# Kernel tuning notes

Hardware: AMD Instinct MI355X
Metric: run time of the kernel (lower is better)

Reference implementation:

```python
import jax, jax.numpy as jnp
import numpy as np

SCALE = 10.0
DIM = 512
DIM_HEAD = 64
HEADS = DIM // DIM_HEAD
LN_EPS = 1e-05
L2_EPS = 1e-12


def l2norm(t, axis=1):
    # Faithful to source: default axis=1 (token axis for [b, n, h, d] tensors)
    denom = jnp.clip(jnp.linalg.norm(t, ord=2, axis=axis, keepdims=True), L2_EPS)
    return t / denom


def setup_inputs() -> dict:
    key = jax.random.key(0)
    k1, k2, k3 = jax.random.split(key, 3)
    B, H, W, C = 8, 32, 32, 512
    x = jax.random.normal(k1, (B, H, W, C), dtype=jnp.float32)
    ln_scale = jnp.ones((C,), dtype=jnp.float32)
    # 1x1 convs == channel matmuls; fan-in scaled init
    w_qkv = jax.random.normal(k2, (C, 3 * DIM), dtype=jnp.float32) / np.sqrt(C)
    w_out = jax.random.normal(k3, (DIM, C), dtype=jnp.float32) / np.sqrt(DIM)
    b_out = jnp.zeros((C,), dtype=jnp.float32)
    return {"x": x, "ln_scale": ln_scale, "w_qkv": w_qkv, "w_out": w_out, "b_out": b_out}


def reference(x, ln_scale, w_qkv, w_out, b_out):
    B, H, W, C = x.shape
    N = H * W
    # LayerNorm over channels (use_bias=False, use_scale=True)
    mean = jnp.mean(x, axis=-1, keepdims=True)
    var = jnp.mean(jnp.square(x - mean), axis=-1, keepdims=True)
    y = (x - mean) * jax.lax.rsqrt(var + LN_EPS) * ln_scale
    # 1x1 conv QKV projection (no bias)
    qkv = jnp.einsum('bhwc,cf->bhwf', y, w_qkv)  # [B,H,W,3*DIM]
    q, k, v = jnp.split(qkv, 3, axis=-1)
    # b x y (h d) -> b (x y) h d
    def to_tokens(t):
        return t.reshape(B, N, HEADS, DIM_HEAD)
    q, k, v = map(to_tokens, (q, k, v))
    # l2norm over axis=1 (token axis), faithful to source default
    q = l2norm(q)
    k = l2norm(k)
    sim = jnp.einsum('bihd,bjhd->bhij', q, k) * SCALE  # [B,heads,N,N]
    attn = jax.nn.softmax(sim, axis=-1)
    out = jnp.einsum('bhij,bjhd->bhid', attn, v)  # [B,heads,N,d]
    # b h (x y) d -> b x y (h d)
    out = out.transpose(0, 2, 1, 3).reshape(B, H, W, HEADS * DIM_HEAD)
    # 1x1 output conv (with bias)
    out = jnp.einsum('bhwf,fc->bhwc', out, w_out) + b_out
    return out
```

## Files before the change

kernel.cpp:

```cpp
#include <hip/hip_runtime.h>

typedef __bf16 bf16x8 __attribute__((ext_vector_type(8)));
typedef float f32x4 __attribute__((ext_vector_type(4)));
typedef float f32x16 __attribute__((ext_vector_type(16)));

#define DEV static __device__ __forceinline__

DEV unsigned short f2bf(float f) {
    union { __bf16 h; unsigned short s; } c; c.h = (__bf16)f; return c.s;
}
DEV float bf2f(unsigned short h) {
    union { unsigned u; float f; } c; c.u = ((unsigned)h) << 16; return c.f;
}
DEV unsigned packbf2(float a, float b) {
    union { __bf16 h[2]; unsigned u; } c;
    c.h[0] = (__bf16)a; c.h[1] = (__bf16)b; return c.u;
}

DEV f32x4 mfma16(bf16x8 a, bf16x8 b, f32x4 c) {
    return __builtin_amdgcn_mfma_f32_16x16x32_bf16(a, b, c, 0, 0, 0);
}
DEV f32x16 mfma32(bf16x8 a, bf16x8 b, f32x16 c) {
    return __builtin_amdgcn_mfma_f32_32x32x16_bf16(a, b, c, 0, 0, 0);
}

#define GLOAD16(gp, lp)                                                        \
    __builtin_amdgcn_global_load_lds(                                          \
        (const __attribute__((address_space(1))) unsigned int*)(gp),           \
        (__attribute__((address_space(3))) unsigned int*)(lp), 16, 0, 0)

#define BARRIER_PINNED()                                                       \
    __builtin_amdgcn_s_barrier();                                              \
    __builtin_amdgcn_sched_barrier(0)

__global__ __launch_bounds__(256) void ln_conv_kernel(const float* __restrict__ x,
                                                      const float* __restrict__ lnsc,
                                                      unsigned short* __restrict__ y,
                                                      float* __restrict__ ssq,
                                                      const float* __restrict__ wqkv,
                                                      const float* __restrict__ wout,
                                                      unsigned short* __restrict__ wqkvt,
                                                      unsigned short* __restrict__ woutt) {
    const int t = threadIdx.x;
    if (blockIdx.x >= 2048) {
        __shared__ __bf16 tile[64][65];
        const int wblk = blockIdx.x - 2048;
        const float* src;
        unsigned short* dst;
        int ldsrc, k0, f0;
        if (wblk < 192) {
            src = wqkv; dst = wqkvt; ldsrc = 1536;
            k0 = (wblk / 24) * 64; f0 = (wblk % 24) * 64;
        } else {
            int w2 = wblk - 192;
            src = wout; dst = woutt; ldsrc = 512;
            k0 = (w2 >> 3) * 64; f0 = (w2 & 7) * 64;
        }
#pragma unroll
        for (int j = 0; j < 16; j++) {
            int idx = t + j * 256;
            int a = idx >> 6, b2 = idx & 63;
            tile[b2][a] = (__bf16)src[(size_t)(k0 + a) * ldsrc + f0 + b2];
        }
        __syncthreads();
#pragma unroll
        for (int j = 0; j < 16; j++) {
            int idx = t + j * 256;
            int fb = idx >> 6, kc = idx & 63;
            union { __bf16 h; unsigned short s; } cv;
            cv.h = tile[fb][kc];
            dst[(size_t)(f0 + fb) * 512 + k0 + kc] = cv.s;
        }
        return;
    }
    if (blockIdx.x < 32) ssq[(blockIdx.x << 8) | t] = 0.0f;
    const int token = blockIdx.x * 4 + (t >> 6);
    const int lane = t & 63;
    const float4* xp = (const float4*)(x + (size_t)token * 512 + lane * 8);
    float4 v0 = xp[0], v1 = xp[1];
    float s = v0.x + v0.y + v0.z + v0.w + v1.x + v1.y + v1.z + v1.w;
    float s2 = v0.x * v0.x + v0.y * v0.y + v0.z * v0.z + v0.w * v0.w +
               v1.x * v1.x + v1.y * v1.y + v1.z * v1.z + v1.w * v1.w;
#pragma unroll
    for (int off = 1; off < 64; off <<= 1) {
        s += __shfl_xor(s, off);
        s2 += __shfl_xor(s2, off);
    }
    const float mean = s * (1.0f / 512.0f);
    const float var = s2 * (1.0f / 512.0f) - mean * mean;
    const float rstd = rsqrtf(var + 1e-5f);
    const float4* sp = (const float4*)(lnsc + lane * 8);
    float4 sc0 = sp[0], sc1 = sp[1];
    union { __bf16 h[8]; uint4 v; } pk;
    pk.h[0] = (__bf16)((v0.x - mean) * rstd * sc0.x);
    pk.h[1] = (__bf16)((v0.y - mean) * rstd * sc0.y);
    pk.h[2] = (__bf16)((v0.z - mean) * rstd * sc0.z);
    pk.h[3] = (__bf16)((v0.w - mean) * rstd * sc0.w);
    pk.h[4] = (__bf16)((v1.x - mean) * rstd * sc1.x);
    pk.h[5] = (__bf16)((v1.y - mean) * rstd * sc1.y);
    pk.h[6] = (__bf16)((v1.z - mean) * rstd * sc1.z);
    pk.h[7] = (__bf16)((v1.w - mean) * rstd * sc1.w);
    *(uint4*)(y + (size_t)token * 512 + lane * 8) = pk.v;
}

template <int WM, int WN, int BK, int NCOLS, bool OUT_BF16, bool BIAS, bool QKV,
          bool DB>
__global__ __launch_bounds__(256) void gemm_bt(const unsigned short* __restrict__ A,
                                               const unsigned short* __restrict__ Bt,
                                               void* __restrict__ Cout,
                                               const float* __restrict__ bias,
                                               float* __restrict__ ssq,
                                               unsigned short* __restrict__ kst,
                                               unsigned short* __restrict__ vst,
                                               int M, int K) {
    constexpr int BM = 2 * WM, BN = 2 * WN;
    constexpr int RB = BK * 2;
    constexpr int RMASK = BK / 8 - 1;
    constexpr int ASZ = BM * RB, BSZ = BN * RB;
    constexpr int NLA = ASZ / 4096, NLB = BSZ / 4096;
    constexpr int MI = WM / 16, NI = WN / 16;
    constexpr int NBUF = DB ? 2 : 1;
    constexpr int STG = NBUF * (ASZ + BSZ);
    constexpr int TTB = QKV ? 128 * 136 * 2 : 0;
    constexpr int LDSB = STG > TTB ? STG : TTB;
    __shared__ __align__(16) char smem[LDSB];
    const int t = threadIdx.x;
    const int w = t >> 6, lane = t & 63;
    const int g = lane >> 4, l15 = lane & 15;
    const int wr = w >> 1, wc = w & 1;
    const int bR = blockIdx.x, bC = blockIdx.y;
    f32x4 acc[MI][NI] = {};
    const size_t ldb = (size_t)K * 2;
    const char* Ag = (const char*)A + (size_t)bR * BM * ldb;
    const char* Bg = (const char*)Bt + (size_t)bC * BN * ldb;

#define GSTAGE(buf, kt_)                                                            \
    {                                                                               \
        char* Ad = smem + (buf) * (ASZ + BSZ);                                      \
        char* Bd = Ad + ASZ;                                                        \
        _Pragma("unroll") for (int i = 0; i < NLA; i++) {                           \
            int o = i * 4096 + t * 16;                                              \
            int row = o / RB, kb = (o % RB) ^ ((row & RMASK) << 4);                 \
            GLOAD16(Ag + (size_t)row * ldb + (size_t)(kt_) * 2 + kb, Ad + o);       \
        }                                                                           \
        _Pragma("unroll") for (int i = 0; i < NLB; i++) {                           \
            int o = i * 4096 + t * 16;                                              \
            int row = o / RB, kb = (o % RB) ^ ((row & RMASK) << 4);                 \
            GLOAD16(Bg + (size_t)row * ldb + (size_t)(kt_) * 2 + kb, Bd + o);       \
        }                                                                           \
    }

#define GCOMPUTE(buf)                                                               \
    {                                                                               \
        const char* Ab = smem + (buf) * (ASZ + BSZ);                                \
        const char* Bb = Ab + ASZ;                                                  \
        _Pragma("unroll") for (int kk = 0; kk < BK; kk += 32) {                     \
            bf16x8 a[MI], bb[NI];                                                   \
            _Pragma("unroll") for (int m = 0; m < MI; m++) {                        \
                int row = wr * WM + m * 16 + l15;                                   \
                int kb = ((kk + g * 8) * 2) ^ ((row & RMASK) << 4);                 \
                a[m] = *(const bf16x8*)(Ab + row * RB + kb);                        \
            }                                                                       \
            _Pragma("unroll") for (int n = 0; n < NI; n++) {                        \
                int row = wc * WN + n * 16 + l15;                                   \
                int kb = ((kk + g * 8) * 2) ^ ((row & RMASK) << 4);                 \
                bb[n] = *(const bf16x8*)(Bb + row * RB + kb);                       \
            }                                                                       \
            _Pragma("unroll") for (int m = 0; m < MI; m++)                          \
                _Pragma("unroll") for (int n = 0; n < NI; n++)                      \
                    acc[m][n] = mfma16(a[m], bb[n], acc[m][n]);                     \
        }                                                                           \
    }

    const int NT = K / BK;
    if constexpr (DB) {
        GSTAGE(0, 0)
        for (int tt = 0; tt < NT; ++tt) {
            const int cur = tt & 1;
            if (tt + 1 < NT) {
                GSTAGE(cur ^ 1, (tt + 1) * BK)
                asm volatile("s_waitcnt vmcnt(%0)" ::"n"(NLA + NLB) : "memory");
            } else {
                asm volatile("s_waitcnt vmcnt(0)" ::: "memory");
            }
            BARRIER_PINNED();
            GCOMPUTE(cur)
            BARRIER_PINNED();
        }
    } else {
        for (int tt = 0; tt < NT; ++tt) {
            __syncthreads();
            GSTAGE(0, tt * BK)
            asm volatile("s_waitcnt vmcnt(0)" ::: "memory");
            __syncthreads();
            GCOMPUTE(0)
        }
    }
#undef GSTAGE
#undef GCOMPUTE

    const int rbase = bR * BM + wr * WM;
    const int cbase = bC * BN + wc * WN;
    if (!QKV || bC < 4) {
#pragma unroll
        for (int m = 0; m < MI; m++)
#pragma unroll
            for (int n = 0; n < NI; n++)
#pragma unroll
                for (int r = 0; r < 4; r++) {
                    int row = rbase + m * 16 + g * 4 + r;
                    int col = cbase + n * 16 + l15;
                    float v = acc[m][n][r];
                    if constexpr (OUT_BF16)
                        ((unsigned short*)Cout)[(size_t)row * NCOLS + col] = f2bf(v);
                    else
                        ((float*)Cout)[(size_t)row * NCOLS + col] =
                            v + (BIAS ? bias[col] : 0.f);
                }
    }
    if constexpr (QKV) {
        if (bC < 8) {
            const int bb2 = bR >> 3;
#pragma unroll
            for (int n = 0; n < NI; n++) {
                float ps = 0.f;
#pragma unroll
                for (int m = 0; m < MI; m++)
#pragma unroll
                    for (int r = 0; r < 4; r++) ps += acc[m][n][r] * acc[m][n][r];
                ps += __shfl_xor(ps, 16);
                ps += __shfl_xor(ps, 32);
                if (g == 0)
                    atomicAdd(&ssq[bb2 * 1024 + cbase + n * 16 + l15], ps);
            }
        }
        if (bC >= 4) {
            unsigned short* TT = (unsigned short*)smem;
            const bool isK = bC < 8;
            __syncthreads();
#pragma unroll
            for (int m = 0; m < MI; m++)
#pragma unroll
                for (int n = 0; n < NI; n++)
#pragma unroll
                    for (int r = 0; r < 4; r++) {
                        int row = wr * WM + m * 16 + g * 4 + r;
                        int col = wc * WN + n * 16 + l15;
                        if (isK)
                            TT[row * 136 + col] = f2bf(acc[m][n][r]);
                        else
                            TT[col * 136 + row] = f2bf(acc[m][n][r]);
                    }
            __syncthreads();
            const int b2 = bR >> 3, rb = bR & 7;
            if (isK) {
#pragma unroll
                for (int j = 0; j < 8; j++) {
                    int sl = (t >> 7) + j * 2;
                    int nl = t & 127;
                    int hh = (bC - 4) * 2 + (sl >> 3), s = sl & 7;
                    *(uint4*)(kst +
                              (((size_t)(b2 * 8 + hh) * 8 + s) * 1024 + rb * 128 + nl) *
                                  8) = *(const uint4*)(TT + nl * 136 + sl * 8);
                }
            } else {
#pragma unroll
                for (int j = 0; j < 8; j++) {
                    int fl = t & 127;
                    int svl = (t >> 7) + j * 2;
                    int hh = (bC - 8) * 2 + (fl >> 6), d = fl & 63;
                    *(uint4*)(vst +
                              (((size_t)(b2 * 8 + hh) * 128 + rb * 16 + svl) * 64 + d) *
                                  8) = *(const uint4*)(TT + fl * 136 + svl * 8);
                }
            }
        }
    }
}

__global__ __launch_bounds__(512, 4) void attn_kernel(
    const unsigned short* __restrict__ qbuf, const unsigned short* __restrict__ kst,
    const unsigned short* __restrict__ vst, unsigned short* __restrict__ attnout,
    const float* __restrict__ ssq) {
    __shared__ __align__(16) char smem[66048];
    float* smq = (float*)(smem + 65536);
    const int t = threadIdx.x, w = t >> 6, lane = t & 63;
    const int hi = lane >> 5, q31 = lane & 31;
    const int g2 = w >> 2, wq = w & 3;
    const int qt = blockIdx.y, bh = blockIdx.x;
    const int b = bh >> 3, h = bh & 7;
    const size_t qrow0 = (size_t)b * 1024 + qt * 128;
    const char* kstb = (const char*)kst + (size_t)bh * 131072;
    const char* vstb = (const char*)vst + (size_t)bh * 131072;

    if (t < 64) {
        float nq = fmaxf(sqrtf(ssq[b * 1024 + h * 64 + t]), 1e-12f);
        float nk = fmaxf(sqrtf(ssq[b * 1024 + 512 + h * 64 + t]), 1e-12f);
        smq[t] = 14.42695040888963f / (nq * nk);
    }
    __syncthreads();

    bf16x8 qf[4];
#pragma unroll
    for (int ds = 0; ds < 4; ds++) {
        union { bf16x8 v; unsigned short u[8]; } in, ov;
        in.v = *(const bf16x8*)(qbuf + (qrow0 + wq * 32 + q31) * 512 + h * 64 +
                                ds * 16 + hi * 8);
#pragma unroll
        for (int j = 0; j < 8; j++)
            ov.u[j] = f2bf(bf2f(in.u[j]) * smq[ds * 16 + hi * 8 + j]);
        qf[ds] = ov.v;
    }

    f32x16 accO[2] = {};
    float prs = 0.f;

#define ASTAGE(buf, tt_)                                                            \
    {                                                                               \
        _Pragma("unroll") for (int i = 0; i < 2; i++) {                             \
            const int c = i * 512 + t;                                              \
            const int hk = c >> 9, sl = (c >> 6) & 7, tl = c & 63;                  \
            GLOAD16(kstb + ((size_t)(sl * 1024 + hk * 512 + (tt_) * 64 + tl) << 4), \
                    smem + (((buf)*2 + hk) << 13) + sl * 1024 + tl * 16);           \
            GLOAD16(vstb + ((size_t)((hk * 64 + (tt_)*8 + sl) * 64 + tl) << 4),     \
                    smem + 32768 + (((buf)*2 + hk) << 13) + sl * 1024 + tl * 16);   \
        }                                                                           \
    }

    ASTAGE(0, 0)
    for (int tt = 0; tt < 8; ++tt) {
        const int cur = tt & 1;
        if (tt < 7) {
            ASTAGE(cur ^ 1, tt + 1)
            asm volatile("s_waitcnt vmcnt(4)" ::: "memory");
        } else {
            asm volatile("s_waitcnt vmcnt(0)" ::: "memory");
        }
        BARRIER_PINNED();
        const char* KsH = smem + ((cur * 2 + g2) << 13);
        const char* VsH = smem + 32768 + ((cur * 2 + g2) << 13);

#pragma unroll
        for (int kvb = 0; kvb < 2; kvb++) {
            f32x16 sa = {};
            __builtin_amdgcn_s_setprio(1);
#pragma unroll
            for (int ds = 0; ds < 4; ds++) {
                bf16x8 kf = *(const bf16x8*)(KsH + ((ds * 2 + hi) << 10) +
                                             ((kvb * 32 + q31) << 4));
                sa = mfma32(kf, qf[ds], sa);
            }
            __builtin_amdgcn_s_setprio(0);
            float p[16];
#pragma unroll
            for (int r = 0; r < 16; r++) {
                p[r] = __builtin_amdgcn_exp2f(sa[r]);
                prs += p[r];
            }
            bf16x8 pf[2];
#pragma unroll
            for (int s2 = 0; s2 < 2; s2++) {
                unsigned a0 = packbf2(p[s2 * 8 + 0], p[s2 * 8 + 1]);
                unsigned a1 = packbf2(p[s2 * 8 + 2], p[s2 * 8 + 3]);
                unsigned b0 = packbf2(p[s2 * 8 + 4], p[s2 * 8 + 5]);
                unsigned b1 = packbf2(p[s2 * 8 + 6], p[s2 * 8 + 7]);
                asm volatile("v_permlane32_swap_b32 %0, %1" : "+v"(a0), "+v"(b0));
                asm volatile("v_permlane32_swap_b32 %0, %1" : "+v"(a1), "+v"(b1));
                union { unsigned u[4]; bf16x8 v; } fr;
                fr.u[0] = a0; fr.u[1] = a1; fr.u[2] = b0; fr.u[3] = b1;
                pf[s2] = fr.v;
            }
            __builtin_amdgcn_s_setprio(1);
#pragma unroll
            for (int s2 = 0; s2 < 2; s2++)
#pragma unroll
                for (int dvb = 0; dvb < 2; dvb++) {
                    bf16x8 vf = *(const bf16x8*)(VsH + ((kvb * 4 + s2 * 2 + hi) << 10) +
                                                 ((dvb * 32 + q31) << 4));
                    accO[dvb] = mfma32(vf, pf[s2], accO[dvb]);
                }
            __builtin_amdgcn_s_setprio(0);
        }
        BARRIER_PINNED();
    }
#undef ASTAGE

    __syncthreads();
    float* comb = (float*)smem;
    float* pe = comb + (wq * 64 + lane) * 36;
    if (g2 == 1) {
        union { f32x16 v; float4 q[4]; } u0, u1;
        u0.v = accO[0]; u1.v = accO[1];
        *(float4*)(pe + 0) = u0.q[0];
        *(float4*)(pe + 4) = u0.q[1];
        *(float4*)(pe + 8) = u0.q[2];
        *(float4*)(pe + 12) = u0.q[3];
        *(float4*)(pe + 16) = u1.q[0];
        *(float4*)(pe + 20) = u1.q[1];
        *(float4*)(pe + 24) = u1.q[2];
        *(float4*)(pe + 28) = u1.q[3];
        pe[32] = prs;
    }
    __syncthreads();
    if (g2 == 0) {
        union { f32x16 v; float4 q[4]; } u0, u1;
        u0.q[0] = *(const float4*)(pe + 0);
        u0.q[1] = *(const float4*)(pe + 4);
        u0.q[2] = *(const float4*)(pe + 8);
        u0.q[3] = *(const float4*)(pe + 12);
        u1.q[0] = *(const float4*)(pe + 16);
        u1.q[1] = *(const float4*)(pe + 20);
        u1.q[2] = *(const float4*)(pe + 24);
        u1.q[3] = *(const float4*)(pe + 28);
        accO[0] += u0.v;
        accO[1] += u1.v;
        prs += pe[32];
        const float tot = prs + __shfl_xor(prs, 32);
        const float inv = 1.0f / tot;
        unsigned short* orow = attnout + (qrow0 + wq * 32 + q31) * 512 + h * 64;
#pragma unroll
        for (int dvb = 0; dvb < 2; dvb++)
#pragma unroll
            for (int grp = 0; grp < 4; grp++) {
                float f0 = accO[dvb][grp * 4 + 0] * inv;
                float f1 = accO[dvb][grp * 4 + 1] * inv;
                float f2 = accO[dvb][grp * 4 + 2] * inv;
                float f3 = accO[dvb][grp * 4 + 3] * inv;
                uint2 pk;
                pk.x = packbf2(f0, f1);
                pk.y = packbf2(f2, f3);
                *(uint2*)(orow + dvb * 32 + grp * 8 + 4 * hi) = pk;
            }
    }
}

extern "C" void kernel_launch(void* const* d_in, const int* in_sizes, int n_in,
                              void* d_out, int out_size, void* d_ws, size_t ws_size,
                              hipStream_t stream) {
    const float* x = (const float*)d_in[0];
    const float* ln_scale = (const float*)d_in[1];
    const float* w_qkv = (const float*)d_in[2];
    const float* w_out = (const float*)d_in[3];
    const float* b_out = (const float*)d_in[4];
    float* out = (float*)d_out;

    char* ws = (char*)d_ws;
    unsigned short* y = (unsigned short*)(ws + 0);
    unsigned short* wqkvt = (unsigned short*)(ws + 8388608);
    unsigned short* woutt = (unsigned short*)(ws + 9961472);
    unsigned short* qbuf = (unsigned short*)(ws + 10485760);
    unsigned short* kst = (unsigned short*)(ws + 18874368);
    unsigned short* vst = (unsigned short*)(ws + 27262976);
    float* ssq = (float*)(ws + 35651584);
    unsigned short* attnout = (unsigned short*)(ws + 0);

    ln_conv_kernel<<<2304, 256, 0, stream>>>(x, ln_scale, y, ssq, w_qkv, w_out, wqkvt,
                                             woutt);
    gemm_bt<64, 64, 64, 512, true, false, true, false>
        <<<dim3(64, 12), 256, 0, stream>>>(y, wqkvt, qbuf, nullptr, ssq, kst, vst,
                                           8192, 512);
    attn_kernel<<<dim3(64, 8), 512, 0, stream>>>(qbuf, kst, vst, attnout, ssq);
    gemm_bt<32, 64, 64, 512, false, true, false, true>
        <<<dim3(128, 4), 256, 0, stream>>>(attnout, woutt, out, b_out, nullptr, nullptr,
                                           nullptr, 8192, 512);
}
```

Baseline: 67.07 us.

## Use three-stage ring-buffered K pipeline with BK=32 for QKV GEMM

```diff
diff --git a/kernel.cpp b/kernel.cpp
--- a/kernel.cpp
+++ b/kernel.cpp
@@ -104,7 +104,7 @@
 }
 
 template <int WM, int WN, int BK, int NCOLS, bool OUT_BF16, bool BIAS, bool QKV,
-          bool DB>
+          bool DB, bool RING>
 __global__ __launch_bounds__(256) void gemm_bt(const unsigned short* __restrict__ A,
                                                const unsigned short* __restrict__ Bt,
                                                void* __restrict__ Cout,
@@ -115,11 +115,10 @@
                                                int M, int K) {
     constexpr int BM = 2 * WM, BN = 2 * WN;
     constexpr int RB = BK * 2;
-    constexpr int RMASK = BK / 8 - 1;
     constexpr int ASZ = BM * RB, BSZ = BN * RB;
     constexpr int NLA = ASZ / 4096, NLB = BSZ / 4096;
     constexpr int MI = WM / 16, NI = WN / 16;
-    constexpr int NBUF = DB ? 2 : 1;
+    constexpr int NBUF = RING ? 3 : (DB ? 2 : 1);
     constexpr int STG = NBUF * (ASZ + BSZ);
     constexpr int TTB = QKV ? 128 * 136 * 2 : 0;
     constexpr int LDSB = STG > TTB ? STG : TTB;
@@ -134,18 +133,20 @@
     const char* Ag = (const char*)A + (size_t)bR * BM * ldb;
     const char* Bg = (const char*)Bt + (size_t)bC * BN * ldb;
 
+#define SWZ(row) (BK == 64 ? (((row)&7) << 4) : ((((row) >> 1) & 3) << 4))
+
 #define GSTAGE(buf, kt_)                                                            \
     {                                                                               \
         char* Ad = smem + (buf) * (ASZ + BSZ);                                      \
         char* Bd = Ad + ASZ;                                                        \
         _Pragma("unroll") for (int i = 0; i < NLA; i++) {                           \
             int o = i * 4096 + t * 16;                                              \
-            int row = o / RB, kb = (o % RB) ^ ((row & RMASK) << 4);                 \
+            int row = o / RB, kb = (o % RB) ^ SWZ(row);                             \
             GLOAD16(Ag + (size_t)row * ldb + (size_t)(kt_) * 2 + kb, Ad + o);       \
         }                                                                           \
         _Pragma("unroll") for (int i = 0; i < NLB; i++) {                           \
             int o = i * 4096 + t * 16;                                              \
-            int row = o / RB, kb = (o % RB) ^ ((row & RMASK) << 4);                 \
+            int row = o / RB, kb = (o % RB) ^ SWZ(row);                             \
             GLOAD16(Bg + (size_t)row * ldb + (size_t)(kt_) * 2 + kb, Bd + o);       \
         }                                                                           \
     }
@@ -158,12 +159,12 @@
             bf16x8 a[MI], bb[NI];                                                   \
             _Pragma("unroll") for (int m = 0; m < MI; m++) {                        \
                 int row = wr * WM + m * 16 + l15;                                   \
-                int kb = ((kk + g * 8) * 2) ^ ((row & RMASK) << 4);                 \
+                int kb = ((kk + g * 8) * 2) ^ SWZ(row);                             \
                 a[m] = *(const bf16x8*)(Ab + row * RB + kb);                        \
             }                                                                       \
             _Pragma("unroll") for (int n = 0; n < NI; n++) {                        \
                 int row = wc * WN + n * 16 + l15;                                   \
-                int kb = ((kk + g * 8) * 2) ^ ((row & RMASK) << 4);                 \
+                int kb = ((kk + g * 8) * 2) ^ SWZ(row);                             \
                 bb[n] = *(const bf16x8*)(Bb + row * RB + kb);                       \
             }                                                                       \
             _Pragma("unroll") for (int m = 0; m < MI; m++)                          \
@@ -173,7 +174,25 @@
     }
 
     const int NT = K / BK;
-    if constexpr (DB) {
+    if constexpr (RING) {
+        GSTAGE(0, 0)
+        GSTAGE(1, BK)
+        int slot = 0;
+        for (int tt = 0; tt < NT; ++tt) {
+            if (tt + 1 < NT) {
+                asm volatile("s_waitcnt vmcnt(%0)" ::"n"(NLA + NLB) : "memory");
+            } else {
+                asm volatile("s_waitcnt vmcnt(0)" ::: "memory");
+            }
+            BARRIER_PINNED();
+            if (tt + 2 < NT) {
+                const int s2 = slot == 0 ? 2 : slot - 1;
+                GSTAGE(s2, (tt + 2) * BK)
+            }
+            GCOMPUTE(slot)
+            slot = slot == 2 ? 0 : slot + 1;
+        }
+    } else if constexpr (DB) {
         GSTAGE(0, 0)
         for (int tt = 0; tt < NT; ++tt) {
             const int cur = tt & 1;
@@ -198,6 +217,7 @@
     }
 #undef GSTAGE
 #undef GCOMPUTE
+#undef SWZ
 
     const int rbase = bR * BM + wr * WM;
     const int cbase = bC * BN + wc * WN;
@@ -456,11 +476,11 @@
 
     ln_conv_kernel<<<2304, 256, 0, stream>>>(x, ln_scale, y, ssq, w_qkv, w_out, wqkvt,
                                              woutt);
-    gemm_bt<64, 64, 64, 512, true, false, true, false>
+    gemm_bt<64, 64, 32, 512, true, false, true, false, true>
         <<<dim3(64, 12), 256, 0, stream>>>(y, wqkvt, qbuf, nullptr, ssq, kst, vst,
                                            8192, 512);
     attn_kernel<<<dim3(64, 8), 512, 0, stream>>>(qbuf, kst, vst, attnout, ssq);
-    gemm_bt<32, 64, 64, 512, false, true, false, true>
+    gemm_bt<32, 64, 64, 512, false, true, false, true, false>
         <<<dim3(128, 4), 256, 0, stream>>>(attnout, woutt, out, b_out, nullptr, nullptr,
                                            nullptr, 8192, 512);
 }
```

After: 68.48 us. +2.1%, slower.
